# Kernel optimization log

Measured on AMD Instinct MI355X. Metric: run time of the kernel, lower is better.

The kernel has to match this reference:

```python
import jax, jax.numpy as jnp
import numpy as np

GAMMA = 2.0
ALPHA = 0.25
EPS = 1e-8
N = 2_000_000


def setup_inputs() -> dict:
    key = jax.random.key(0)
    k1, k2, k3, k4, k5, k6 = jax.random.split(key, 6)
    return {
        "kl_logits": jax.random.normal(k1, (N, 4), dtype=jnp.float32),
        "jsnm_logits": jax.random.normal(k2, (N, 3), dtype=jnp.float32),
        "jsnl_logits": jax.random.normal(k3, (N, 3), dtype=jnp.float32),
        "class_weights": jax.random.uniform(k4, (5,), dtype=jnp.float32),
        "kl_t": jax.random.randint(k5, (N,), 0, 5, dtype=jnp.int32),
        "jsnm_t": jax.random.randint(k6, (N,), 0, 4, dtype=jnp.int32),
        "jsnl_t": jax.random.randint(jax.random.fold_in(key, 7), (N,), 0, 4, dtype=jnp.int32),
    }


def _coral_focal_loss(logits, targets, class_weights, kl_labels):
    # logits: [B, K-1]; targets: [B] ordinal labels in 0..K-1
    km1 = logits.shape[1]
    prob = jax.nn.sigmoid(logits)
    # vectorized CORAL target matrix: row i has ones in columns < targets[i]
    tm = (jnp.arange(km1)[None, :] < targets[:, None]).astype(logits.dtype)  # [B, K-1]
    pt = jnp.where(tm == 1, prob, 1.0 - prob)
    focal_weight = (1.0 - pt) ** GAMMA
    alpha_t = jnp.where(tm == 1, ALPHA, 1.0 - ALPHA)
    ce = tm * jnp.log(prob + EPS) + (1.0 - tm) * jnp.log(1.0 - prob + EPS)
    loss = -alpha_t * focal_weight * ce  # [B, K-1]
    # per-sample weight gathered by the KL label (as in the torch code)
    loss = loss * class_weights[kl_labels][:, None]
    return jnp.mean(loss)


def reference(kl_logits, jsnm_logits, jsnl_logits, class_weights, kl_t, jsnm_t, jsnl_t):
    l_kl = _coral_focal_loss(kl_logits, kl_t, class_weights, kl_t)
    l_jsnm = _coral_focal_loss(jsnm_logits, jsnm_t, class_weights, kl_t)
    l_jsnl = _coral_focal_loss(jsnl_logits, jsnl_t, class_weights, kl_t)
    total = (l_kl + l_jsnm + l_jsnl) / 3.0
    return total, l_kl, l_jsnm, l_jsnl
```

## Files before the change

### kernel.cpp

```cpp
#include <hip/hip_runtime.h>

constexpr int THREADS = 256;
constexpr int WAVES   = THREADS / 64;

#define NLOG2E -1.44269504088896340f
#define C_TM1   0.17328679513998632f
#define C_TM0   0.51986038541995900f

__device__ __forceinline__ float coral_term(float x, bool tm) {
    float y  = tm ? x : -x;
    float e  = __builtin_amdgcn_exp2f(y * NLOG2E);
    float d  = 1.0f + e;
    float r  = __builtin_amdgcn_rcpf(d);
    float om = e * r;
    float L  = __builtin_amdgcn_logf(d);
    float w  = tm ? C_TM1 : C_TM0;
    return om * om * w * L;
}

__device__ __forceinline__ void do_sample(
        float kx, float ky, float kz, float kw,
        float ma, float mb, float mc,
        float la, float lb, float lc,
        int kt, int mt, int lt, float w,
        float& s0, float& s1, float& s2) {
    float a = coral_term(kx, 0 < kt) + coral_term(ky, 1 < kt)
            + coral_term(kz, 2 < kt) + coral_term(kw, 3 < kt);
    s0 = fmaf(w, a, s0);
    float b = coral_term(ma, 0 < mt) + coral_term(mb, 1 < mt)
            + coral_term(mc, 2 < mt);
    s1 = fmaf(w, b, s1);
    float c = coral_term(la, 0 < lt) + coral_term(lb, 1 < lt)
            + coral_term(lc, 2 < lt);
    s2 = fmaf(w, c, s2);
}

__global__ __launch_bounds__(THREADS) void coral_main(
        const float* __restrict__ kl_logits,
        const float* __restrict__ jsnm_logits,
        const float* __restrict__ jsnl_logits,
        const float* __restrict__ cw,
        const int*   __restrict__ kl_t,
        const int*   __restrict__ jsnm_t,
        const int*   __restrict__ jsnl_t,
        float*       __restrict__ partials,
        int n, int ngroups) {
    __shared__ float lw[8];
    if (threadIdx.x < 5) lw[threadIdx.x] = cw[threadIdx.x];
    __syncthreads();

    float s0 = 0.0f, s1 = 0.0f, s2 = 0.0f;

    const int stride = gridDim.x * THREADS;
    const float4* kl4 = reinterpret_cast<const float4*>(kl_logits);
    const float4* m4  = reinterpret_cast<const float4*>(jsnm_logits);
    const float4* l4  = reinterpret_cast<const float4*>(jsnl_logits);
    const int4*   kt4 = reinterpret_cast<const int4*>(kl_t);
    const int4*   mt4 = reinterpret_cast<const int4*>(jsnm_t);
    const int4*   lt4 = reinterpret_cast<const int4*>(jsnl_t);

    for (int g = blockIdx.x * THREADS + threadIdx.x; g < ngroups; g += stride) {
        const int4 kt = kt4[g];
        const int4 mt = mt4[g];
        const int4 lt = lt4[g];
        const float wx = lw[kt.x];
        const float wy = lw[kt.y];
        const float wz = lw[kt.z];
        const float ww = lw[kt.w];

        const float4 k0 = kl4[4 * g + 0];
        const float4 k1 = kl4[4 * g + 1];
        const float4 k2 = kl4[4 * g + 2];
        const float4 k3 = kl4[4 * g + 3];
        const float4 m0 = m4[3 * g + 0];
        const float4 m1 = m4[3 * g + 1];
        const float4 m2 = m4[3 * g + 2];
        const float4 l0 = l4[3 * g + 0];
        const float4 l1 = l4[3 * g + 1];
        const float4 l2 = l4[3 * g + 2];

        do_sample(k0.x, k0.y, k0.z, k0.w, m0.x, m0.y, m0.z, l0.x, l0.y, l0.z,
                  kt.x, mt.x, lt.x, wx, s0, s1, s2);
        do_sample(k1.x, k1.y, k1.z, k1.w, m0.w, m1.x, m1.y, l0.w, l1.x, l1.y,
                  kt.y, mt.y, lt.y, wy, s0, s1, s2);
        do_sample(k2.x, k2.y, k2.z, k2.w, m1.z, m1.w, m2.x, l1.z, l1.w, l2.x,
                  kt.z, mt.z, lt.z, wz, s0, s1, s2);
        do_sample(k3.x, k3.y, k3.z, k3.w, m2.y, m2.z, m2.w, l2.y, l2.z, l2.w,
                  kt.w, mt.w, lt.w, ww, s0, s1, s2);
    }

    const int tail_base = ngroups << 2;
    for (int i = tail_base + blockIdx.x * THREADS + threadIdx.x; i < n;
         i += stride) {
        do_sample(kl_logits[4 * i], kl_logits[4 * i + 1], kl_logits[4 * i + 2],
                  kl_logits[4 * i + 3],
                  jsnm_logits[3 * i], jsnm_logits[3 * i + 1], jsnm_logits[3 * i + 2],
                  jsnl_logits[3 * i], jsnl_logits[3 * i + 1], jsnl_logits[3 * i + 2],
                  kl_t[i], jsnm_t[i], jsnl_t[i], lw[kl_t[i]], s0, s1, s2);
    }

    #pragma unroll
    for (int off = 32; off > 0; off >>= 1) {
        s0 += __shfl_xor(s0, off);
        s1 += __shfl_xor(s1, off);
        s2 += __shfl_xor(s2, off);
    }

    __shared__ float red[3][WAVES];
    const int lane = threadIdx.x & 63;
    const int wid  = threadIdx.x >> 6;
    if (lane == 0) {
        red[0][wid] = s0;
        red[1][wid] = s1;
        red[2][wid] = s2;
    }
    __syncthreads();
    if (threadIdx.x == 0) {
        float t0 = 0.0f, t1 = 0.0f, t2 = 0.0f;
        #pragma unroll
        for (int wv = 0; wv < WAVES; ++wv) {
            t0 += red[0][wv];
            t1 += red[1][wv];
            t2 += red[2][wv];
        }
        partials[blockIdx.x * 3 + 0] = t0;
        partials[blockIdx.x * 3 + 1] = t1;
        partials[blockIdx.x * 3 + 2] = t2;
    }
}

__global__ __launch_bounds__(THREADS) void coral_finalize(
        const float* __restrict__ partials, float* __restrict__ out,
        int nblocks, float n) {
    float s0 = 0.0f, s1 = 0.0f, s2 = 0.0f;
    for (int i = threadIdx.x; i < nblocks; i += THREADS) {
        s0 += partials[3 * i + 0];
        s1 += partials[3 * i + 1];
        s2 += partials[3 * i + 2];
    }
    #pragma unroll
    for (int off = 32; off > 0; off >>= 1) {
        s0 += __shfl_xor(s0, off);
        s1 += __shfl_xor(s1, off);
        s2 += __shfl_xor(s2, off);
    }
    __shared__ float red[3][WAVES];
    const int lane = threadIdx.x & 63;
    const int wid  = threadIdx.x >> 6;
    if (lane == 0) {
        red[0][wid] = s0;
        red[1][wid] = s1;
        red[2][wid] = s2;
    }
    __syncthreads();
    if (threadIdx.x == 0) {
        float t0 = 0.0f, t1 = 0.0f, t2 = 0.0f;
        #pragma unroll
        for (int wv = 0; wv < WAVES; ++wv) {
            t0 += red[0][wv];
            t1 += red[1][wv];
            t2 += red[2][wv];
        }
        const float l_kl   = t0 / (n * 4.0f);
        const float l_jsnm = t1 / (n * 3.0f);
        const float l_jsnl = t2 / (n * 3.0f);
        out[0] = (l_kl + l_jsnm + l_jsnl) / 3.0f;
        out[1] = l_kl;
        out[2] = l_jsnm;
        out[3] = l_jsnl;
    }
}

extern "C" void kernel_launch(void* const* d_in, const int* in_sizes, int n_in,
                              void* d_out, int out_size, void* d_ws, size_t ws_size,
                              hipStream_t stream) {
    const float* kl_logits   = (const float*)d_in[0];
    const float* jsnm_logits = (const float*)d_in[1];
    const float* jsnl_logits = (const float*)d_in[2];
    const float* cw          = (const float*)d_in[3];
    const int*   kl_t        = (const int*)d_in[4];
    const int*   jsnm_t      = (const int*)d_in[5];
    const int*   jsnl_t      = (const int*)d_in[6];
    const int n = in_sizes[4];

    const int ngroups = n >> 2;
    int blocks = (ngroups + THREADS - 1) / THREADS;
    if (blocks < 1) blocks = 1;

    float* partials = (float*)d_ws;
    float* out      = (float*)d_out;

    coral_main<<<blocks, THREADS, 0, stream>>>(
        kl_logits, jsnm_logits, jsnl_logits, cw, kl_t, jsnm_t, jsnl_t,
        partials, n, ngroups);
    coral_finalize<<<1, THREADS, 0, stream>>>(partials, out, blocks, (float)n);
}
```

Measured before the change: 26.96 us.

## Fuse final reduction into main kernel via last-block atomic counter

```diff
diff --git a/kernel.cpp b/kernel.cpp
--- a/kernel.cpp
+++ b/kernel.cpp
@@ -1,6 +1,6 @@
 #include <hip/hip_runtime.h>
 
-constexpr int THREADS = 256;
+constexpr int THREADS = 512;
 constexpr int WAVES   = THREADS / 64;
 
 #define NLOG2E -1.44269504088896340f
@@ -35,7 +35,7 @@
     s2 = fmaf(w, c, s2);
 }
 
-__global__ __launch_bounds__(THREADS) void coral_main(
+__global__ __launch_bounds__(THREADS) void coral_fused(
         const float* __restrict__ kl_logits,
         const float* __restrict__ jsnm_logits,
         const float* __restrict__ jsnl_logits,
@@ -43,8 +43,10 @@
         const int*   __restrict__ kl_t,
         const int*   __restrict__ jsnm_t,
         const int*   __restrict__ jsnl_t,
+        unsigned*    __restrict__ counter,
         float*       __restrict__ partials,
-        int n, int ngroups) {
+        float*       __restrict__ out,
+        int n, int ngroups, int nblocks, float fn) {
     __shared__ float lw[8];
     if (threadIdx.x < 5) lw[threadIdx.x] = cw[threadIdx.x];
     __syncthreads();
@@ -115,6 +117,8 @@
         red[2][wid] = s2;
     }
     __syncthreads();
+
+    __shared__ bool amLast;
     if (threadIdx.x == 0) {
         float t0 = 0.0f, t1 = 0.0f, t2 = 0.0f;
         #pragma unroll
@@ -126,31 +130,32 @@
         partials[blockIdx.x * 3 + 0] = t0;
         partials[blockIdx.x * 3 + 1] = t1;
         partials[blockIdx.x * 3 + 2] = t2;
-    }
-}
-
-__global__ __launch_bounds__(THREADS) void coral_finalize(
-        const float* __restrict__ partials, float* __restrict__ out,
-        int nblocks, float n) {
-    float s0 = 0.0f, s1 = 0.0f, s2 = 0.0f;
+        __threadfence();
+        unsigned old = atomicAdd(counter, 1u);
+        amLast = (old == (unsigned)(nblocks - 1));
+    }
+    __syncthreads();
+
+    if (!amLast) return;
+
+    __threadfence();
+    float f0 = 0.0f, f1 = 0.0f, f2 = 0.0f;
     for (int i = threadIdx.x; i < nblocks; i += THREADS) {
-        s0 += partials[3 * i + 0];
-        s1 += partials[3 * i + 1];
-        s2 += partials[3 * i + 2];
+        f0 += partials[3 * i + 0];
+        f1 += partials[3 * i + 1];
+        f2 += partials[3 * i + 2];
     }
     #pragma unroll
     for (int off = 32; off > 0; off >>= 1) {
-        s0 += __shfl_xor(s0, off);
-        s1 += __shfl_xor(s1, off);
-        s2 += __shfl_xor(s2, off);
-    }
-    __shared__ float red[3][WAVES];
-    const int lane = threadIdx.x & 63;
-    const int wid  = threadIdx.x >> 6;
+        f0 += __shfl_xor(f0, off);
+        f1 += __shfl_xor(f1, off);
+        f2 += __shfl_xor(f2, off);
+    }
+    __syncthreads();
     if (lane == 0) {
-        red[0][wid] = s0;
-        red[1][wid] = s1;
-        red[2][wid] = s2;
+        red[0][wid] = f0;
+        red[1][wid] = f1;
+        red[2][wid] = f2;
     }
     __syncthreads();
     if (threadIdx.x == 0) {
@@ -161,9 +166,9 @@
             t1 += red[1][wv];
             t2 += red[2][wv];
         }
-        const float l_kl   = t0 / (n * 4.0f);
-        const float l_jsnm = t1 / (n * 3.0f);
-        const float l_jsnl = t2 / (n * 3.0f);
+        const float l_kl   = t0 / (fn * 4.0f);
+        const float l_jsnm = t1 / (fn * 3.0f);
+        const float l_jsnl = t2 / (fn * 3.0f);
         out[0] = (l_kl + l_jsnm + l_jsnl) / 3.0f;
         out[1] = l_kl;
         out[2] = l_jsnm;
@@ -187,11 +192,12 @@
     int blocks = (ngroups + THREADS - 1) / THREADS;
     if (blocks < 1) blocks = 1;
 
-    float* partials = (float*)d_ws;
-    float* out      = (float*)d_out;
-
-    coral_main<<<blocks, THREADS, 0, stream>>>(
+    unsigned* counter  = (unsigned*)d_ws;
+    float*    partials = (float*)((char*)d_ws + 256);
+    float*    out      = (float*)d_out;
+
+    hipMemsetAsync(counter, 0, sizeof(unsigned), stream);
+    coral_fused<<<blocks, THREADS, 0, stream>>>(
         kl_logits, jsnm_logits, jsnl_logits, cw, kl_t, jsnm_t, jsnl_t,
-        partials, n, ngroups);
-    coral_finalize<<<1, THREADS, 0, stream>>>(partials, out, blocks, (float)n);
-}
+        counter, partials, out, n, ngroups, blocks, (float)n);
+}
```

Measured after the change: 59.30 us. 2.2x slower.
